# Performance work log

Hardware: AMD Instinct MI355X
Metric: run time of the kernel (lower is better)

Reference implementation:

```python
import jax, jax.numpy as jnp
import numpy as np

N = 50000      # nodes
E = 800000     # edges (before self-loops)
F_IN = 128     # num_features
H = 4          # heads
C = 64         # hidden_channels
HC = H * C     # 256
NEG_SLOPE = 0.2


def setup_inputs() -> dict:
    key = jax.random.key(0)
    ks = jax.random.split(key, 20)
    x = jax.random.normal(ks[0], (N, F_IN), dtype=jnp.float32)
    edge_index = jax.random.randint(ks[1], (2, E), 0, N, dtype=jnp.int32)
    s = 0.05
    inp = {"x": x, "edge_index": edge_index}
    dims_in = [F_IN, HC, HC, HC]
    for l in range(4):
        kW, ka, kb = jax.random.split(ks[2 + l], 3)
        inp[f"W{l+1}"] = jax.random.normal(kW, (dims_in[l], HC), dtype=jnp.float32) * s
        inp[f"a_src{l+1}"] = jax.random.normal(ka, (H, C), dtype=jnp.float32) * s
        inp[f"a_dst{l+1}"] = jax.random.normal(kb, (H, C), dtype=jnp.float32) * s
        inp[f"b{l+1}"] = jnp.zeros((HC,), dtype=jnp.float32)
    return inp


def gat_conv(x, src, dst, W, a_src, a_dst, b):
    # x: [N, F_in] -> h: [N, H, C]
    h = (x @ W).reshape(N, H, C)
    es = jnp.sum(h * a_src, axis=-1)  # [N, H] per-node source logits
    ed = jnp.sum(h * a_dst, axis=-1)  # [N, H]
    e = jax.nn.leaky_relu(es[src] + ed[dst], NEG_SLOPE)  # [Etot, H]
    m = jax.ops.segment_max(e, dst, num_segments=N)      # per-dst max
    m = jnp.where(jnp.isfinite(m), m, 0.0)
    ex = jnp.exp(e - m[dst])
    denom = jax.ops.segment_sum(ex, dst, num_segments=N)
    alpha = ex / (denom[dst] + 1e-16)                     # edge softmax
    out = jax.ops.segment_sum(alpha[:, :, None] * h[src], dst, num_segments=N)
    return out.reshape(N, HC) + b


def reference(x, edge_index,
              W1, a_src1, a_dst1, b1,
              W2, a_src2, a_dst2, b2,
              W3, a_src3, a_dst3, b3,
              W4, a_src4, a_dst4, b4):
    loop = jnp.arange(N, dtype=edge_index.dtype)
    src = jnp.concatenate([edge_index[0], loop])  # add self-loops (PyG default)
    dst = jnp.concatenate([edge_index[1], loop])
    x1 = jax.nn.relu(gat_conv(x, src, dst, W1, a_src1, a_dst1, b1))
    x2 = jax.nn.relu(gat_conv(x1, src, dst, W2, a_src2, a_dst2, b2))
    x3 = jax.nn.relu(gat_conv(x2 + x1, src, dst, W3, a_src3, a_dst3, b3))
    x4 = jax.nn.relu(gat_conv(x2 + x3, src, dst, W4, a_src4, a_dst4, b4))
    # NOTE: source code calls conv4 again (not conv5) -- reproduced faithfully
    x5 = gat_conv(x4 + x3, src, dst, W4, a_src4, a_dst4, b4)
    return x5
```

## Files before the change

### kernel.cpp

```cpp
#include <hip/hip_runtime.h>
#include <hip/hip_bf16.h>

#define N_NODES 50000
#define E_EDGES 800000
#define ETOT (E_EDGES + N_NODES)
#define HC 256
#define NHEAD 4
#define CHAN 64
#define NEG 0.2f
#define NBLK ((N_NODES + 1023) / 1024)

typedef _Float16 half8 __attribute__((ext_vector_type(8)));
typedef _Float16 half4v __attribute__((ext_vector_type(4)));
typedef float float4v __attribute__((ext_vector_type(4)));


__global__ void count_kernel(const int* __restrict__ ei, int* __restrict__ counts) {
    int i = blockIdx.x * blockDim.x + threadIdx.x;
    if (i >= ETOT) return;
    int dst = (i < E_EDGES) ? ei[E_EDGES + i] : (i - E_EDGES);
    atomicAdd(&counts[dst], 1);
}

__global__ __launch_bounds__(256) void blocksum_kernel(const int* __restrict__ counts,
                                                       int* __restrict__ blocksums) {
    __shared__ int s[4];
    int b = blockIdx.x, tid = threadIdx.x;
    int base = b * 1024;
    int sum = 0;
    #pragma unroll
    for (int r = 0; r < 4; ++r) {
        int idx = base + r * 256 + tid;
        sum += (idx < N_NODES) ? counts[idx] : 0;
    }
    #pragma unroll
    for (int m = 1; m < 64; m <<= 1) sum += __shfl_xor(sum, m, 64);
    if ((tid & 63) == 0) s[tid >> 6] = sum;
    __syncthreads();
    if (tid == 0) blocksums[b] = s[0] + s[1] + s[2] + s[3];
}

__global__ __launch_bounds__(64) void blockscan_kernel(int* __restrict__ blocksums) {
    int tid = threadIdx.x;
    int v = (tid < NBLK) ? blocksums[tid] : 0;
    #pragma unroll
    for (int off = 1; off < 64; off <<= 1) {
        int t = __shfl_up(v, off, 64);
        if (tid >= off) v += t;
    }
    if (tid < NBLK) blocksums[tid] = v;
}

__global__ __launch_bounds__(1024) void scatter_scan_kernel(const int* __restrict__ counts,
                                                            const int* __restrict__ blocksums,
                                                            int* __restrict__ offsets,
                                                            int* __restrict__ cursor) {
    __shared__ int s[1024];
    int b = blockIdx.x, tid = threadIdx.x;
    int idx = b * 1024 + tid;
    int v = (idx < N_NODES) ? counts[idx] : 0;
    s[tid] = v;
    __syncthreads();
    for (int off = 1; off < 1024; off <<= 1) {
        int t = (tid >= off) ? s[tid - off] : 0;
        __syncthreads();
        s[tid] += t;
        __syncthreads();
    }
    int excl = s[tid] - v + (b > 0 ? blocksums[b - 1] : 0);
    if (idx < N_NODES) { offsets[idx] = excl; cursor[idx] = excl; }
    if (idx == N_NODES - 1) offsets[N_NODES] = excl + v;
}

__global__ void fill_kernel(const int* __restrict__ ei, int* __restrict__ cursor,
                            int2* __restrict__ csr) {
    int i = blockIdx.x * blockDim.x + threadIdx.x;
    if (i >= ETOT) return;
    int src, dst;
    if (i < E_EDGES) { src = ei[i]; dst = ei[E_EDGES + i]; }
    else             { src = i - E_EDGES; dst = src; }
    int pos = atomicAdd(&cursor[dst], 1);
    csr[pos] = make_int2(src, dst);
}


__global__ void wsplit_kernel(const float* __restrict__ W, _Float16* __restrict__ Wth,
                              _Float16* __restrict__ Wtl, int K) {
    int id = blockIdx.x * 256 + threadIdx.x;
    if (id >= K * 256) return;
    int n = id & 255, k = id >> 8;
    float w = W[(size_t)k * 256 + n];
    _Float16 h = (_Float16)w;
    _Float16 l = (_Float16)(w - (float)h);
    Wth[(size_t)n * K + k] = h;
    Wtl[(size_t)n * K + k] = l;
}

__global__ void xsplit_kernel(const float* __restrict__ x, _Float16* __restrict__ xh,
                              _Float16* __restrict__ xl, int total) {
    int id = blockIdx.x * 256 + threadIdx.x;
    if (id >= total) return;
    float v = x[id];
    _Float16 h = (_Float16)v;
    xh[id] = h;
    xl[id] = (_Float16)(v - (float)h);
}


__global__ __launch_bounds__(256) void edge_alpha_kernel(
        const float* __restrict__ es, const float* __restrict__ ed,
        const int2* __restrict__ csr, float* __restrict__ ex) {
    int e = blockIdx.x * 256 + threadIdx.x;
    if (e >= ETOT) return;
    int2 sd = csr[e];
    float4 esv = *(const float4*)(es + (size_t)sd.x * 4);
    float4 edv = *(const float4*)(ed + (size_t)sd.y * 4);
    float4 v;
    v.x = esv.x + edv.x; v.y = esv.y + edv.y;
    v.z = esv.z + edv.z; v.w = esv.w + edv.w;
    v.x = (v.x > 0.f) ? v.x : NEG * v.x;
    v.y = (v.y > 0.f) ? v.y : NEG * v.y;
    v.z = (v.z > 0.f) ? v.z : NEG * v.z;
    v.w = (v.w > 0.f) ? v.w : NEG * v.w;
    v.x = __expf(v.x); v.y = __expf(v.y);
    v.z = __expf(v.z); v.w = __expf(v.w);
    *(float4*)(ex + (size_t)e * 4) = v;
}


template<int K, bool HASLO>
struct SmemLayout {
    _Float16 Ah[64][K + 8];
    _Float16 Al[HASLO ? 64 : 1][HASLO ? (K + 8) : 8];
    _Float16 Bh[256][40];
    _Float16 Bl[256][40];
};
template<int K, bool HASLO>
union SmemU {
    SmemLayout<K, HASLO> t;
    _Float16 out[64][264];
};

template<int K, bool HASLO, bool HAS2>
__global__ __launch_bounds__(256) void gemm_mfma_kernel(
        const _Float16* __restrict__ A1h, const _Float16* __restrict__ A1l,
        const _Float16* __restrict__ A2h,
        const _Float16* __restrict__ Wth, const _Float16* __restrict__ Wtl,
        const float* __restrict__ a_src, const float* __restrict__ a_dst,
        _Float16* __restrict__ H16, float* __restrict__ es, float* __restrict__ ed,
        int M) {
    constexpr int NC  = K / 32;
    constexpr int CPR = K / 8;
    __shared__ SmemU<K, HASLO> u;
    auto& Ah = u.t.Ah;
    auto& Al = u.t.Al;
    auto& Bh = u.t.Bh;
    auto& Bl = u.t.Bl;

    int tid = threadIdx.x;
    int m0 = blockIdx.x * 64;
    int w = tid >> 6, lane = tid & 63;
    int rn = w * 64;
    int fr = lane & 15;
    int q  = lane >> 4;
    int fk = q * 8;

    int wr = tid >> 2;
    int wk = (tid & 3) * 8;

    half8 a1c[NC], a2c[HAS2 ? NC : 1], alc[HASLO ? NC : 1];
    #pragma unroll
    for (int c = 0; c < NC; ++c) {
        int idx = c * 256 + tid;
        int row = idx / CPR, col = (idx % CPR) * 8;
        int grow = m0 + row;
        a1c[c] = (half8)(_Float16)0;
        if (grow < M) a1c[c] = *(const half8*)(A1h + (size_t)grow * K + col);
        if constexpr (HAS2) {
            a2c[c] = (half8)(_Float16)0;
            if (grow < M) a2c[c] = *(const half8*)(A2h + (size_t)grow * K + col);
        }
        if constexpr (HASLO) {
            alc[c] = (half8)(_Float16)0;
            if (grow < M) alc[c] = *(const half8*)(A1l + (size_t)grow * K + col);
        }
    }
    half8 pbh[4], pbl[4];
    auto loadB = [&](int k0) {
        #pragma unroll
        for (int g = 0; g < 4; ++g) {
            int r = g * 64 + wr;
            pbh[g] = *(const half8*)(Wth + (size_t)r * K + k0 + wk);
            pbl[g] = *(const half8*)(Wtl + (size_t)r * K + k0 + wk);
        }
    };
    loadB(0);

    #pragma unroll
    for (int c = 0; c < NC; ++c) {
        int idx = c * 256 + tid;
        int row = idx / CPR, col = (idx % CPR) * 8;
        half8 v = a1c[c];
        if constexpr (HAS2) v = v + a2c[c];
        *(half8*)&Ah[row][col] = v;
        if constexpr (HASLO) *(half8*)&Al[row][col] = alc[c];
    }

    float4v acc[4][4];
    #pragma unroll
    for (int i = 0; i < 4; ++i)
        #pragma unroll
        for (int j = 0; j < 4; ++j)
            acc[i][j] = (float4v){0.f, 0.f, 0.f, 0.f};

    __syncthreads();

    for (int kk = 0; kk < K / 32; ++kk) {
        int k0 = kk * 32;
        #pragma unroll
        for (int g = 0; g < 4; ++g) {
            int r = g * 64 + wr;
            *(half8*)&Bh[r][wk] = pbh[g];
            *(half8*)&Bl[r][wk] = pbl[g];
        }
        __syncthreads();
        if (kk + 1 < K / 32) loadB(k0 + 32);
        half8 afh[4], bfh[4], bfl[4];
        #pragma unroll
        for (int t = 0; t < 4; ++t) {
            afh[t] = *(const half8*)&Ah[t * 16 + fr][k0 + fk];
            bfh[t] = *(const half8*)&Bh[rn + t * 16 + fr][fk];
            bfl[t] = *(const half8*)&Bl[rn + t * 16 + fr][fk];
        }
        if constexpr (HASLO) {
            half8 afl[4];
            #pragma unroll
            for (int t = 0; t < 4; ++t) afl[t] = *(const half8*)&Al[t * 16 + fr][k0 + fk];
            #pragma unroll
            for (int tm = 0; tm < 4; ++tm)
                #pragma unroll
                for (int tn = 0; tn < 4; ++tn)
                    acc[tm][tn] = __builtin_amdgcn_mfma_f32_16x16x32_f16(
                        afl[tm], bfh[tn], acc[tm][tn], 0, 0, 0);
        }
        #pragma unroll
        for (int tm = 0; tm < 4; ++tm)
            #pragma unroll
            for (int tn = 0; tn < 4; ++tn) {
                float4v c = acc[tm][tn];
                c = __builtin_amdgcn_mfma_f32_16x16x32_f16(afh[tm], bfl[tn], c, 0, 0, 0);
                c = __builtin_amdgcn_mfma_f32_16x16x32_f16(afh[tm], bfh[tn], c, 0, 0, 0);
                acc[tm][tn] = c;
            }
        __syncthreads();
    }

    float asv[4], adv[4];
    #pragma unroll
    for (int tn = 0; tn < 4; ++tn) {
        asv[tn] = a_src[w * CHAN + tn * 16 + fr];
        adv[tn] = a_dst[w * CHAN + tn * 16 + fr];
    }
    #pragma unroll
    for (int tm = 0; tm < 4; ++tm) {
        #pragma unroll
        for (int i = 0; i < 4; ++i) {
            int r = tm * 16 + q * 4 + i;
            float ps = 0.f, pd = 0.f;
            #pragma unroll
            for (int tn = 0; tn < 4; ++tn) {
                float hv = acc[tm][tn][i];
                ps += hv * asv[tn];
                pd += hv * adv[tn];
                u.out[r][rn + tn * 16 + fr] = (_Float16)hv;
            }
            #pragma unroll
            for (int msk = 1; msk < 16; msk <<= 1) {
                ps += __shfl_xor(ps, msk, 64);
                pd += __shfl_xor(pd, msk, 64);
            }
            int row = m0 + r;
            if (fr == 0 && row < M) {
                es[row * NHEAD + w] = ps;
                ed[row * NHEAD + w] = pd;
            }
        }
    }
    __syncthreads();

    #pragma unroll
    for (int k = 0; k < 8; ++k) {
        int c = k * 256 + tid;
        int r = c >> 5, cc = c & 31;
        if (m0 + r < M) {
            half8 v = *(const half8*)(&u.out[r][0] + cc * 8);
            *(half8*)(H16 + (size_t)(m0 + r) * HC + cc * 8) = v;
        }
    }
}


__global__ __launch_bounds__(256) void gat_aggregate_kernel(
        const _Float16* __restrict__ H16, const float* __restrict__ ex,
        const int* __restrict__ offsets, const int2* __restrict__ csr,
        const float* __restrict__ bias, _Float16* __restrict__ out16,
        float* __restrict__ out32, int do_relu) {
    __shared__ float ex_lds[4][256];
    __shared__ int   src_lds[4][64];
    int tid = threadIdx.x;
    int w = tid >> 6, lane = tid & 63;
    int n = blockIdx.x * 4 + w;
    int off = offsets[n];
    int deg = offsets[n + 1] - off;

    if (deg <= 64) {
        int sreg = n;
        float4 ex4 = make_float4(0.f, 0.f, 0.f, 0.f);
        if (lane < deg) {
            sreg = csr[off + lane].x;
            ex4 = *(const float4*)(ex + (size_t)(off + lane) * 4);
        }
        src_lds[w][lane] = sreg;
        *(float4*)&ex_lds[w][lane * 4] = ex4;

        int hl = lane & 31, side = lane >> 5;
        int hd = hl >> 3;
        float av[8] = {0.f, 0.f, 0.f, 0.f, 0.f, 0.f, 0.f, 0.f};
        int degr = (deg + 7) & ~7;
        #pragma unroll 2
        for (int j0 = 0; j0 < degr; j0 += 8) {
            int j = j0 + side;
            int s0 = src_lds[w][j];
            int s1 = src_lds[w][j + 2];
            int s2 = src_lds[w][j + 4];
            int s3 = src_lds[w][j + 6];
            float w0 = ex_lds[w][j * 4 + hd];
            float w1 = ex_lds[w][(j + 2) * 4 + hd];
            float w2 = ex_lds[w][(j + 4) * 4 + hd];
            float w3 = ex_lds[w][(j + 6) * 4 + hd];
            half8 h0 = *(const half8*)(H16 + (size_t)s0 * HC + hl * 8);
            half8 h1 = *(const half8*)(H16 + (size_t)s1 * HC + hl * 8);
            half8 h2 = *(const half8*)(H16 + (size_t)s2 * HC + hl * 8);
            half8 h3 = *(const half8*)(H16 + (size_t)s3 * HC + hl * 8);
            #pragma unroll
            for (int c = 0; c < 8; ++c) {
                av[c] += w0 * (float)h0[c];
                av[c] += w1 * (float)h1[c];
                av[c] += w2 * (float)h2[c];
                av[c] += w3 * (float)h3[c];
            }
        }

        float4 l4 = ex4;
        #pragma unroll
        for (int msk = 1; msk < 64; msk <<= 1) {
            l4.x += __shfl_xor(l4.x, msk, 64);
            l4.y += __shfl_xor(l4.y, msk, 64);
            l4.z += __shfl_xor(l4.z, msk, 64);
            l4.w += __shfl_xor(l4.w, msk, 64);
        }
        #pragma unroll
        for (int c = 0; c < 8; ++c) av[c] += __shfl_xor(av[c], 32, 64);
        if (side == 0) {
            float denom = (hd == 0) ? l4.x : (hd == 1) ? l4.y : (hd == 2) ? l4.z : l4.w;
            float scale = 1.f / (denom + 1e-16f);
            float4 b0 = *(const float4*)(bias + hl * 8);
            float4 b1 = *(const float4*)(bias + hl * 8 + 4);
            float o[8] = {av[0] * scale + b0.x, av[1] * scale + b0.y,
                          av[2] * scale + b0.z, av[3] * scale + b0.w,
                          av[4] * scale + b1.x, av[5] * scale + b1.y,
                          av[6] * scale + b1.z, av[7] * scale + b1.w};
            if (do_relu)
                #pragma unroll
                for (int c = 0; c < 8; ++c) o[c] = fmaxf(o[c], 0.f);
            if (out16) {
                half8 ov = {(_Float16)o[0], (_Float16)o[1], (_Float16)o[2], (_Float16)o[3],
                            (_Float16)o[4], (_Float16)o[5], (_Float16)o[6], (_Float16)o[7]};
                *(half8*)(out16 + (size_t)n * HC + hl * 8) = ov;
            } else {
                *(float4*)(out32 + (size_t)n * HC + hl * 8) =
                    make_float4(o[0], o[1], o[2], o[3]);
                *(float4*)(out32 + (size_t)n * HC + hl * 8 + 4) =
                    make_float4(o[4], o[5], o[6], o[7]);
            }
        }
        return;
    }

    int head = lane >> 4;
    float4 acc0 = make_float4(0.f, 0.f, 0.f, 0.f);
    float den = 0.f;
    for (int j = 0; j < deg; ++j) {
        int s = csr[off + j].x;
        float exv = ex[(size_t)(off + j) * 4 + head];
        den += exv;
        half4v h0 = *(const half4v*)(H16 + (size_t)s * HC + lane * 4);
        acc0.x += exv * (float)h0[0]; acc0.y += exv * (float)h0[1];
        acc0.z += exv * (float)h0[2]; acc0.w += exv * (float)h0[3];
    }
    float scale = 1.f / (den + 1e-16f);
    float4 b4 = *(const float4*)(bias + lane * 4);
    float o[4] = {acc0.x * scale + b4.x, acc0.y * scale + b4.y,
                  acc0.z * scale + b4.z, acc0.w * scale + b4.w};
    if (do_relu)
        #pragma unroll
        for (int c = 0; c < 4; ++c) o[c] = fmaxf(o[c], 0.f);
    if (out16) {
        half4v ov = {(_Float16)o[0], (_Float16)o[1], (_Float16)o[2], (_Float16)o[3]};
        *(half4v*)(out16 + (size_t)n * HC + lane * 4) = ov;
    } else {
        *(float4*)(out32 + (size_t)n * HC + lane * 4) = make_float4(o[0], o[1], o[2], o[3]);
    }
}


extern "C" void kernel_launch(void* const* d_in, const int* in_sizes, int n_in,
                              void* d_out, int out_size, void* d_ws, size_t ws_size,
                              hipStream_t stream) {
    const float* x  = (const float*)d_in[0];
    const int*   ei = (const int*)d_in[1];
    const float *W[5], *Asrc[5], *Adst[5], *Bs[5];
    for (int l = 0; l < 4; ++l) {
        W[l]    = (const float*)d_in[2 + l * 4];
        Asrc[l] = (const float*)d_in[3 + l * 4];
        Adst[l] = (const float*)d_in[4 + l * 4];
        Bs[l]   = (const float*)d_in[5 + l * 4];
    }
    W[4] = W[3]; Asrc[4] = Asrc[3]; Adst[4] = Adst[3]; Bs[4] = Bs[3];

    char* ws = (char*)d_ws;
    size_t off = 0;
    auto alloc = [&](size_t bytes) -> void* {
        void* p = ws + off;
        off += (bytes + 255) & ~(size_t)255;
        return p;
    };
    _Float16* h16  = (_Float16*)alloc((size_t)N_NODES * HC * 2);
    _Float16* xa   = (_Float16*)alloc((size_t)N_NODES * HC * 2);
    _Float16* xb   = (_Float16*)alloc((size_t)N_NODES * HC * 2);
    _Float16* xc   = (_Float16*)alloc((size_t)N_NODES * HC * 2);
    _Float16* xd   = (_Float16*)alloc((size_t)N_NODES * HC * 2);
    _Float16* xh   = (_Float16*)alloc((size_t)N_NODES * 128 * 2);
    _Float16* xl   = (_Float16*)alloc((size_t)N_NODES * 128 * 2);
    float* es      = (float*)alloc((size_t)N_NODES * 4 * 4);
    float* ed      = (float*)alloc((size_t)N_NODES * 4 * 4);
    float* exbuf   = (float*)alloc((size_t)ETOT * 4 * 4);
    int*   counts  = (int*)alloc((size_t)N_NODES * 4);
    int*   offsets = (int*)alloc((size_t)(N_NODES + 1) * 4);
    int*   cursor  = (int*)alloc((size_t)N_NODES * 4);
    int2*  csr     = (int2*)alloc((size_t)ETOT * 8);
    int*   blocksums = (int*)alloc((size_t)NBLK * 4);
    _Float16 *Wth[5], *Wtl[5];
    int Ks[4] = {128, 256, 256, 256};
    for (int l = 0; l < 4; ++l) {
        Wth[l] = (_Float16*)alloc((size_t)256 * Ks[l] * 2);
        Wtl[l] = (_Float16*)alloc((size_t)256 * Ks[l] * 2);
    }
    Wth[4] = Wth[3]; Wtl[4] = Wtl[3];

    hipMemsetAsync(counts, 0, (size_t)N_NODES * 4, stream);
    count_kernel<<<(ETOT + 255) / 256, 256, 0, stream>>>(ei, counts);
    blocksum_kernel<<<NBLK, 256, 0, stream>>>(counts, blocksums);
    blockscan_kernel<<<1, 64, 0, stream>>>(blocksums);
    scatter_scan_kernel<<<NBLK, 1024, 0, stream>>>(counts, blocksums, offsets, cursor);
    fill_kernel<<<(ETOT + 255) / 256, 256, 0, stream>>>(ei, cursor, csr);
    for (int l = 0; l < 4; ++l)
        wsplit_kernel<<<(Ks[l] * 256 + 255) / 256, 256, 0, stream>>>(W[l], Wth[l], Wtl[l], Ks[l]);
    xsplit_kernel<<<(N_NODES * 128 + 255) / 256, 256, 0, stream>>>(x, xh, xl, N_NODES * 128);

    int gemm_grid = (N_NODES + 63) / 64;
    auto agg = [&](int l, _Float16* o16, float* o32, int relu) {
        edge_alpha_kernel<<<(ETOT + 255) / 256, 256, 0, stream>>>(
            es, ed, csr, exbuf);
        gat_aggregate_kernel<<<N_NODES / 4, 256, 0, stream>>>(
            h16, exbuf, offsets, csr, Bs[l], o16, o32, relu);
    };

    float* out = (float*)d_out;
    gemm_mfma_kernel<128, true, false><<<gemm_grid, 256, 0, stream>>>(
        xh, xl, nullptr, Wth[0], Wtl[0], Asrc[0], Adst[0], h16, es, ed, N_NODES);
    agg(0, xa, nullptr, 1);
    gemm_mfma_kernel<256, false, false><<<gemm_grid, 256, 0, stream>>>(
        xa, nullptr, nullptr, Wth[1], Wtl[1], Asrc[1], Adst[1], h16, es, ed, N_NODES);
    agg(1, xb, nullptr, 1);
    gemm_mfma_kernel<256, false, true><<<gemm_grid, 256, 0, stream>>>(
        xb, nullptr, xa, Wth[2], Wtl[2], Asrc[2], Adst[2], h16, es, ed, N_NODES);
    agg(2, xc, nullptr, 1);
    gemm_mfma_kernel<256, false, true><<<gemm_grid, 256, 0, stream>>>(
        xb, nullptr, xc, Wth[3], Wtl[3], Asrc[3], Adst[3], h16, es, ed, N_NODES);
    agg(3, xd, nullptr, 1);
    gemm_mfma_kernel<256, false, true><<<gemm_grid, 256, 0, stream>>>(
        xd, nullptr, xc, Wth[4], Wtl[4], Asrc[4], Adst[4], h16, es, ed, N_NODES);
    agg(4, nullptr, out, 0);
}
```

Baseline: 749.1 us.

## Store edge weights in fp16, merge weight splits, split aggregate launches

Edge exp weights are now stored as half4 instead of float4, which halves the write traffic in edge_alpha and the read traffic in the aggregate kernel. The four weight-split launches are merged into one kernel, removing three launches. The aggregate kernel is split into two launches over node halves via a node_base offset, which only adds a launch. The fp16 exp values lose precision and could overflow if a logit exceeds about 11, since there is no max subtraction.

```diff
diff --git a/kernel.cpp b/kernel.cpp
--- a/kernel.cpp
+++ b/kernel.cpp
@@ -84,16 +84,26 @@
 }
 
 
-__global__ void wsplit_kernel(const float* __restrict__ W, _Float16* __restrict__ Wth,
-                              _Float16* __restrict__ Wtl, int K) {
+__global__ __launch_bounds__(256) void wsplit_all_kernel(
+        const float* __restrict__ W0, const float* __restrict__ W1,
+        const float* __restrict__ W2, const float* __restrict__ W3,
+        _Float16* __restrict__ Th0, _Float16* __restrict__ Tl0,
+        _Float16* __restrict__ Th1, _Float16* __restrict__ Tl1,
+        _Float16* __restrict__ Th2, _Float16* __restrict__ Tl2,
+        _Float16* __restrict__ Th3, _Float16* __restrict__ Tl3) {
     int id = blockIdx.x * 256 + threadIdx.x;
-    if (id >= K * 256) return;
+    const float* W; _Float16 *Th, *Tl; int K;
+    if (id < 32768)       { W = W0; Th = Th0; Tl = Tl0; K = 128; }
+    else if (id < 98304)  { W = W1; Th = Th1; Tl = Tl1; K = 256; id -= 32768; }
+    else if (id < 163840) { W = W2; Th = Th2; Tl = Tl2; K = 256; id -= 98304; }
+    else if (id < 229376) { W = W3; Th = Th3; Tl = Tl3; K = 256; id -= 163840; }
+    else return;
     int n = id & 255, k = id >> 8;
     float w = W[(size_t)k * 256 + n];
     _Float16 h = (_Float16)w;
     _Float16 l = (_Float16)(w - (float)h);
-    Wth[(size_t)n * K + k] = h;
-    Wtl[(size_t)n * K + k] = l;
+    Th[(size_t)n * K + k] = h;
+    Tl[(size_t)n * K + k] = l;
 }
 
 __global__ void xsplit_kernel(const float* __restrict__ x, _Float16* __restrict__ xh,
@@ -109,7 +119,7 @@
 
 __global__ __launch_bounds__(256) void edge_alpha_kernel(
         const float* __restrict__ es, const float* __restrict__ ed,
-        const int2* __restrict__ csr, float* __restrict__ ex) {
+        const int2* __restrict__ csr, _Float16* __restrict__ ex) {
     int e = blockIdx.x * 256 + threadIdx.x;
     if (e >= ETOT) return;
     int2 sd = csr[e];
@@ -122,9 +132,9 @@
     v.y = (v.y > 0.f) ? v.y : NEG * v.y;
     v.z = (v.z > 0.f) ? v.z : NEG * v.z;
     v.w = (v.w > 0.f) ? v.w : NEG * v.w;
-    v.x = __expf(v.x); v.y = __expf(v.y);
-    v.z = __expf(v.z); v.w = __expf(v.w);
-    *(float4*)(ex + (size_t)e * 4) = v;
+    half4v o = {(_Float16)__expf(v.x), (_Float16)__expf(v.y),
+                (_Float16)__expf(v.z), (_Float16)__expf(v.w)};
+    *(half4v*)(ex + (size_t)e * 4) = o;
 }
 
 
@@ -301,25 +311,26 @@
 
 
 __global__ __launch_bounds__(256) void gat_aggregate_kernel(
-        const _Float16* __restrict__ H16, const float* __restrict__ ex,
+        const _Float16* __restrict__ H16, const _Float16* __restrict__ ex,
         const int* __restrict__ offsets, const int2* __restrict__ csr,
         const float* __restrict__ bias, _Float16* __restrict__ out16,
-        float* __restrict__ out32, int do_relu) {
+        float* __restrict__ out32, int do_relu, int node_base) {
     __shared__ float ex_lds[4][256];
     __shared__ int   src_lds[4][64];
     int tid = threadIdx.x;
     int w = tid >> 6, lane = tid & 63;
-    int n = blockIdx.x * 4 + w;
+    int n = node_base + blockIdx.x * 4 + w;
     int off = offsets[n];
     int deg = offsets[n + 1] - off;
 
     if (deg <= 64) {
         int sreg = n;
-        float4 ex4 = make_float4(0.f, 0.f, 0.f, 0.f);
+        half4v exh = (half4v)(_Float16)0;
         if (lane < deg) {
             sreg = csr[off + lane].x;
-            ex4 = *(const float4*)(ex + (size_t)(off + lane) * 4);
-        }
+            exh = *(const half4v*)(ex + (size_t)(off + lane) * 4);
+        }
+        float4 ex4 = make_float4((float)exh[0], (float)exh[1], (float)exh[2], (float)exh[3]);
         src_lds[w][lane] = sreg;
         *(float4*)&ex_lds[w][lane * 4] = ex4;
 
@@ -392,7 +403,7 @@
     float den = 0.f;
     for (int j = 0; j < deg; ++j) {
         int s = csr[off + j].x;
-        float exv = ex[(size_t)(off + j) * 4 + head];
+        float exv = (float)ex[(size_t)(off + j) * 4 + head];
         den += exv;
         half4v h0 = *(const half4v*)(H16 + (size_t)s * HC + lane * 4);
         acc0.x += exv * (float)h0[0]; acc0.y += exv * (float)h0[1];
@@ -444,7 +455,7 @@
     _Float16* xl   = (_Float16*)alloc((size_t)N_NODES * 128 * 2);
     float* es      = (float*)alloc((size_t)N_NODES * 4 * 4);
     float* ed      = (float*)alloc((size_t)N_NODES * 4 * 4);
-    float* exbuf   = (float*)alloc((size_t)ETOT * 4 * 4);
+    _Float16* exbuf = (_Float16*)alloc((size_t)ETOT * 4 * 2);
     int*   counts  = (int*)alloc((size_t)N_NODES * 4);
     int*   offsets = (int*)alloc((size_t)(N_NODES + 1) * 4);
     int*   cursor  = (int*)alloc((size_t)N_NODES * 4);
@@ -464,16 +475,19 @@
     blockscan_kernel<<<1, 64, 0, stream>>>(blocksums);
     scatter_scan_kernel<<<NBLK, 1024, 0, stream>>>(counts, blocksums, offsets, cursor);
     fill_kernel<<<(ETOT + 255) / 256, 256, 0, stream>>>(ei, cursor, csr);
-    for (int l = 0; l < 4; ++l)
-        wsplit_kernel<<<(Ks[l] * 256 + 255) / 256, 256, 0, stream>>>(W[l], Wth[l], Wtl[l], Ks[l]);
+    wsplit_all_kernel<<<(229376 + 255) / 256, 256, 0, stream>>>(
+        W[0], W[1], W[2], W[3],
+        Wth[0], Wtl[0], Wth[1], Wtl[1], Wth[2], Wtl[2], Wth[3], Wtl[3]);
     xsplit_kernel<<<(N_NODES * 128 + 255) / 256, 256, 0, stream>>>(x, xh, xl, N_NODES * 128);
 
     int gemm_grid = (N_NODES + 63) / 64;
     auto agg = [&](int l, _Float16* o16, float* o32, int relu) {
         edge_alpha_kernel<<<(ETOT + 255) / 256, 256, 0, stream>>>(
             es, ed, csr, exbuf);
-        gat_aggregate_kernel<<<N_NODES / 4, 256, 0, stream>>>(
-            h16, exbuf, offsets, csr, Bs[l], o16, o32, relu);
+        gat_aggregate_kernel<<<N_NODES / 8, 256, 0, stream>>>(
+            h16, exbuf, offsets, csr, Bs[l], o16, o32, relu, 0);
+        gat_aggregate_kernel<<<N_NODES / 8, 256, 0, stream>>>(
+            h16, exbuf, offsets, csr, Bs[l], o16, o32, relu, N_NODES / 2);
     };
 
     float* out = (float*)d_out;
```

New measurement: 764.5 us. 1.02x slower.
